# Kernel optimization log

Measured on AMD Instinct MI355X. Metric: run time of the kernel, lower is better.

## Reference

```python
import jax, jax.numpy as jnp
import numpy as np

BN_EPS = 1e-5

def conv1x1(t, w, b):
    # t: [B,Cin,H,W], w: [Cout,Cin], b: [Cout]
    return jnp.einsum('bchw,oc->bohw', t, w) + b[None, :, None, None]

def setup_inputs() -> dict:
    key = jax.random.key(0)
    ks = jax.random.split(key, 11)
    B, Cx, Hx, Wx = 8, 64, 128, 64
    Cy, Hy, Wy = 256, 64, 32
    d = Cy // 8  # num_heads=8
    return {
        'x': jax.random.normal(ks[0], (B, Cx, Hx, Wx), jnp.float32),
        'y': jax.random.normal(ks[1], (B, Cy, Hy, Wy), jnp.float32),
        'wq': jax.random.normal(ks[2], (d, Cy), jnp.float32) * 0.05,
        'bq': jax.random.normal(ks[3], (d,), jnp.float32) * 0.05,
        'wk': jax.random.normal(ks[4], (d, Cy), jnp.float32) * 0.05,
        'bk': jax.random.normal(ks[5], (d,), jnp.float32) * 0.05,
        'wv': jax.random.normal(ks[6], (Cx, Cx), jnp.float32) * 0.05,
        'bv': jax.random.normal(ks[7], (Cx,), jnp.float32) * 0.05,
        'gamma': jax.random.normal(ks[8], (1,), jnp.float32),
        'bn_w': jax.random.normal(ks[9], (Cx,), jnp.float32),
        'bn_b': jax.random.normal(ks[10], (Cx,), jnp.float32),
    }

def reference(x, y, wq, bq, wk, bk, wv, bv, gamma, bn_w, bn_b):
    B, Cx, Hx, Wx = x.shape
    _, Cy, Hy, Wy = y.shape
    size_x = Hx * Wx
    size_y = Hy * Wy
    r = size_x // size_y  # nearest-upsample replication factor (integer here)

    q = conv1x1(y, wq, bq).reshape(B, -1, size_y)  # [B,d,Sy]
    k = conv1x1(y, wk, bk).reshape(B, -1, size_y)  # [B,d,Sy]
    energy = jnp.einsum('bds,bdt->bst', q, k)      # [B,Sy,Sy]
    A = jax.nn.softmax(energy, axis=-1)            # [B,Sy,Sy]

    v = conv1x1(x, wv, bv).reshape(B, Cx, size_x)  # [B,Cx,Sx]
    # Nearest upsample of A to [Sx,Sx] with A_up[i,j]=A[i//r, j//r], then
    # out[c,i] = sum_j v[c,j]*A_up[i,j]  ==  repeat( v_pooled @ A^T , r )
    v_pool = v.reshape(B, Cx, size_y, r).sum(-1)   # block-sum over j within each low-res bin
    O = jnp.einsum('bcj,bij->bci', v_pool, A)      # [B,Cx,Sy]
    out = jnp.repeat(O, r, axis=-1)                # replicate along i: index i -> i//r
    out = out.reshape(B, Cx, Hx, Wx)

    out = gamma[0] * out
    # BatchNorm2d (training-mode batch statistics, biased variance)
    mean = out.mean(axis=(0, 2, 3), keepdims=True)
    var = out.var(axis=(0, 2, 3), keepdims=True)
    out = (out - mean) * jax.lax.rsqrt(var + BN_EPS)
    out = out * bn_w[None, :, None, None] + bn_b[None, :, None, None]
    return x + out
```

## Files before the change

kernel.cpp:

```cpp
#include <hip/hip_runtime.h>
#include <hip/hip_bf16.h>

typedef __attribute__((ext_vector_type(8))) short short8;
typedef __attribute__((ext_vector_type(4))) float f32x4;
typedef unsigned short ushort_t;
typedef unsigned int uint_t;

static constexpr int B  = 8;
static constexpr int CX = 64;
static constexpr int SX = 8192;
static constexpr int CY = 256;
static constexpr int SY = 2048;
static constexpr int D  = 32;

static constexpr size_t OFF_Q  = 0;
static constexpr size_t OFF_K  = OFF_Q + (size_t)B*SY*D*2;
static constexpr size_t OFF_V  = OFF_K + (size_t)B*SY*D*2;
static constexpr size_t OFF_O  = OFF_V + (size_t)B*CX*SY*2;
static constexpr size_t OFF_P1 = OFF_O + (size_t)B*CX*SY*4;
static constexpr size_t OFF_P2 = OFF_P1 + 512*64*4;
static constexpr size_t OFF_SC = OFF_P2 + 512*64*4;
static constexpr size_t OFF_SH = OFF_SC + 64*4;

__device__ inline ushort_t f2bf(float f) {
    uint_t u = __builtin_bit_cast(uint_t, f);
    u += 0x7fffu + ((u >> 16) & 1u);
    return (ushort_t)(u >> 16);
}
__device__ inline uint_t pack_bf16(float a, float b) {
    uint_t ua = __builtin_bit_cast(uint_t, a);
    uint_t ub = __builtin_bit_cast(uint_t, b);
    ua += 0x7fffu + ((ua >> 16) & 1u);
    ub += 0x7fffu + ((ub >> 16) & 1u);
    return (ua >> 16) | (ub & 0xffff0000u);
}

__global__ __launch_bounds__(1024) void k_qk(
    const float* __restrict__ y, const float* __restrict__ wq,
    const float* __restrict__ bq, const float* __restrict__ wk,
    const float* __restrict__ bk, ushort_t* __restrict__ qT, ushort_t* __restrict__ kT)
{
    __shared__ __align__(16) unsigned char Wl[32768];
    __shared__ __align__(16) unsigned char Yl[32768];
    const int t  = threadIdx.x;
    const int b  = blockIdx.x >> 5;
    const int s0 = (blockIdx.x & 31) << 6;

#pragma unroll
    for (int p = 0; p < 8; ++p) {
        const int idx = p * 1024 + t;
        const int o   = idx >> 7;
        const int c2  = idx & 127;
        const float f0 = (o < 32) ? wq[o * CY + 2 * c2]     : wk[(o - 32) * CY + 2 * c2];
        const float f1 = (o < 32) ? wq[o * CY + 2 * c2 + 1] : wk[(o - 32) * CY + 2 * c2 + 1];
        *reinterpret_cast<uint_t*>(Wl + ((o * 512 + c2 * 4) ^ ((o & 7) << 4))) = pack_bf16(f0, f1);
    }
    {
        const int l = t & 63, cg = t >> 6;
        const float* ysrc = y + (size_t)(b * CY + cg * 16) * SY + s0 + l;
#pragma unroll
        for (int k = 0; k < 8; ++k) {
            const float f0 = ysrc[(2 * k)     * SY];
            const float f1 = ysrc[(2 * k + 1) * SY];
            const int c = cg * 16 + 2 * k;
            *reinterpret_cast<uint_t*>(Yl + ((l * 512 + c * 2) ^ ((l & 7) << 4))) = pack_bf16(f0, f1);
        }
    }
    __syncthreads();

    const int w  = t >> 6, l = t & 63;
    const int li = l & 15, g = l >> 4;
    const int ot = w & 3,  st = w >> 2;
    const int oo = ot * 16 + li;
    const int ss = st * 16 + li;

    f32x4 acc = (f32x4){0.f, 0.f, 0.f, 0.f};
#pragma unroll
    for (int ch = 0; ch < 8; ++ch) {
        const short8 wf = *reinterpret_cast<const short8*>(
            Wl + ((oo * 512 + ch * 64 + g * 16) ^ ((oo & 7) << 4)));
        const short8 yf = *reinterpret_cast<const short8*>(
            Yl + ((ss * 512 + ch * 64 + g * 16) ^ ((ss & 7) << 4)));
        acc = __builtin_amdgcn_mfma_f32_16x16x32_bf16(wf, yf, acc, 0, 0, 0);
    }
    const float* bias = (ot < 2) ? bq : bk;
    const int ob = (ot & 1) * 16 + g * 4;
    const float v0 = acc[0] + bias[ob + 0];
    const float v1 = acc[1] + bias[ob + 1];
    const float v2 = acc[2] + bias[ob + 2];
    const float v3 = acc[3] + bias[ob + 3];
    uint2 pw; pw.x = pack_bf16(v0, v1); pw.y = pack_bf16(v2, v3);
    ushort_t* dst = (ot < 2) ? qT : kT;
    *reinterpret_cast<uint2*>(dst + (size_t)(b * SY + s0 + ss) * D + ob) = pw;
}

__global__ __launch_bounds__(1024) void k_v(
    const float* __restrict__ x, const float* __restrict__ wv,
    const float* __restrict__ bv, ushort_t* __restrict__ vB)
{
    __shared__ __align__(16) float xp[64][68];
    __shared__ __align__(16) float wt[64][68];
    const int t   = threadIdx.x;
    const int b   = blockIdx.x >> 5;
    const int jj0 = (blockIdx.x & 31) << 6;

#pragma unroll
    for (int p = 0; p < 4; ++p) {
        const int f = p * 1024 + t;
        const int co = f >> 6, ci = f & 63;
        wt[ci][co] = wv[co * 64 + ci];
    }
    {
        const float4* x4 = reinterpret_cast<const float4*>(x);
#pragma unroll
        for (int p = 0; p < 4; ++p) {
            const int f = p * 1024 + t;
            const int ci = f >> 6, j = f & 63;
            const float4 v = x4[(size_t)(b * CX + ci) * (SX / 4) + jj0 + j];
            xp[ci][j] = (v.x + v.y) + (v.z + v.w);
        }
    }
    __syncthreads();

    const int w = t >> 6, j = t & 63;
    float a0 = 0.f, a1 = 0.f, a2 = 0.f, a3 = 0.f;
#pragma unroll 4
    for (int ci = 0; ci < 64; ++ci) {
        const float xv = xp[ci][j];
        const float4 w4 = *reinterpret_cast<const float4*>(&wt[ci][w * 4]);
        a0 += w4.x * xv; a1 += w4.y * xv; a2 += w4.z * xv; a3 += w4.w * xv;
    }
    const int c0 = w * 4;
    const size_t base = (size_t)(b * CX) * SY + jj0 + j;
    vB[base + (size_t)(c0 + 0) * SY] = f2bf(a0 + 4.f * bv[c0 + 0]);
    vB[base + (size_t)(c0 + 1) * SY] = f2bf(a1 + 4.f * bv[c0 + 1]);
    vB[base + (size_t)(c0 + 2) * SY] = f2bf(a2 + 4.f * bv[c0 + 2]);
    vB[base + (size_t)(c0 + 3) * SY] = f2bf(a3 + 4.f * bv[c0 + 3]);
}

__global__ __launch_bounds__(1024) void k_attn(
    const ushort_t* __restrict__ qT, const ushort_t* __restrict__ kT,
    const ushort_t* __restrict__ vB, float* __restrict__ O,
    float* __restrict__ part1, float* __restrict__ part2)
{
    __shared__ __align__(16) unsigned char smem[65536];
    unsigned char* Kb0 = smem;
    unsigned char* Kb1 = smem + 8192;
    unsigned char* Vb0 = smem + 16384;
    unsigned char* Vb1 = smem + 32768;
    unsigned char* Pl  = smem + 49152;
    float* Otile = reinterpret_cast<float*>(smem);
    float* Lpart = reinterpret_cast<float*>(smem + 17408);
    float* invL  = reinterpret_cast<float*>(smem + 19456);

    const int t  = threadIdx.x;
    const int w  = t >> 6, l = t & 63;
    const int g  = l >> 4, li = l & 15;
    const int b  = blockIdx.x >> 5;
    const int i0 = (blockIdx.x & 31) << 6;

    const int jtt = w >> 1, h = w & 1;
    const int n   = w & 3,  ks = w >> 2;
    const int m0  = 2 * h, m1 = 2 * h + 1;

    const ushort_t* kb = kT + (size_t)b * SY * D;
    const ushort_t* vb = vB + (size_t)b * CX * SY;

    const short8 qf0 = *reinterpret_cast<const short8*>(
        qT + ((size_t)(b * SY + i0 + m0 * 16 + li)) * D + g * 8);
    const short8 qf1 = *reinterpret_cast<const short8*>(
        qT + ((size_t)(b * SY + i0 + m1 * 16 + li)) * D + g * 8);

    const int koff = w * 1024 + l * 16;
    const int vc = w * 4 + g;
    const int vldso = vc * 256 + li * 16;
    const unsigned char* kgb = reinterpret_cast<const unsigned char*>(kb);
    const unsigned char* vgb = reinterpret_cast<const unsigned char*>(vb)
                             + (size_t)vc * (SY * 2) + ((li ^ (vc & 7)) * 16);

    f32x4 acc[4];
#pragma unroll
    for (int m = 0; m < 4; ++m) acc[m] = (f32x4){0.f, 0.f, 0.f, 0.f};
    float lsum0 = 0.f, lsum1 = 0.f;

    const int swzP = (li & 7) << 4;

    {
        short8 kr, vr;
        if (w < 8) kr = *reinterpret_cast<const short8*>(kgb + koff);
        vr = *reinterpret_cast<const short8*>(vgb);
        if (w < 8) *reinterpret_cast<short8*>(Kb0 + koff) = kr;
        *reinterpret_cast<short8*>(Vb0 + vldso) = vr;
    }
    __syncthreads();

    for (int ch = 0; ch < 16; ++ch) {
        unsigned char* Kc = (ch & 1) ? Kb1 : Kb0;
        unsigned char* Vc = (ch & 1) ? Vb1 : Vb0;
        unsigned char* Kn = (ch & 1) ? Kb0 : Kb1;
        unsigned char* Vn = (ch & 1) ? Vb0 : Vb1;

        short8 kr, vr;
        if (ch < 15) {
            if (w < 8) kr = *reinterpret_cast<const short8*>(kgb + (size_t)(ch + 1) * 8192 + koff);
            vr = *reinterpret_cast<const short8*>(vgb + (size_t)(ch + 1) * 256);
        }

        const short8 kf = *reinterpret_cast<const short8*>(Kc + (jtt * 16 + li) * 64 + g * 16);
        const f32x4 d0 = __builtin_amdgcn_mfma_f32_16x16x32_bf16(kf, qf0, (f32x4){0.f,0.f,0.f,0.f}, 0, 0, 0);
        const f32x4 d1 = __builtin_amdgcn_mfma_f32_16x16x32_bf16(kf, qf1, (f32x4){0.f,0.f,0.f,0.f}, 0, 0, 0);

        {
            const float e0 = __expf(d0[0]), e1 = __expf(d0[1]);
            const float e2 = __expf(d0[2]), e3 = __expf(d0[3]);
            lsum0 += (e0 + e1) + (e2 + e3);
            uint2 pw; pw.x = pack_bf16(e0, e1); pw.y = pack_bf16(e2, e3);
            *reinterpret_cast<uint2*>(Pl + (m0 * 16 + li) * 256 + ((jtt * 32 + g * 8) ^ swzP)) = pw;
        }
        {
            const float e0 = __expf(d1[0]), e1 = __expf(d1[1]);
            const float e2 = __expf(d1[2]), e3 = __expf(d1[3]);
            lsum1 += (e0 + e1) + (e2 + e3);
            uint2 pw; pw.x = pack_bf16(e0, e1); pw.y = pack_bf16(e2, e3);
            *reinterpret_cast<uint2*>(Pl + (m1 * 16 + li) * 256 + ((jtt * 32 + g * 8) ^ swzP)) = pw;
        }
        __syncthreads();

        const short8 vf = *reinterpret_cast<const short8*>(
            Vc + (n * 16 + li) * 256 + ((ks * 64 + g * 16) ^ swzP));
#pragma unroll
        for (int m = 0; m < 4; ++m) {
            const short8 pf = *reinterpret_cast<const short8*>(
                Pl + (m * 16 + li) * 256 + ((ks * 64 + g * 16) ^ swzP));
            acc[m] = __builtin_amdgcn_mfma_f32_16x16x32_bf16(pf, vf, acc[m], 0, 0, 0);
        }

        if (ch < 15) {
            if (w < 8) *reinterpret_cast<short8*>(Kn + koff) = kr;
            *reinterpret_cast<short8*>(Vn + vldso) = vr;
        }
        __syncthreads();
    }

    lsum0 += __shfl_xor(lsum0, 16, 64);
    lsum0 += __shfl_xor(lsum0, 32, 64);
    lsum1 += __shfl_xor(lsum1, 16, 64);
    lsum1 += __shfl_xor(lsum1, 32, 64);
    if (l < 16) {
        Lpart[jtt * 64 + m0 * 16 + l] = lsum0;
        Lpart[jtt * 64 + m1 * 16 + l] = lsum1;
    }
    if (ks == 0) {
#pragma unroll
        for (int m = 0; m < 4; ++m) {
            float4 v = make_float4(acc[m][0], acc[m][1], acc[m][2], acc[m][3]);
            *reinterpret_cast<float4*>(&Otile[(n * 16 + li) * 68 + m * 16 + g * 4]) = v;
        }
    }
    __syncthreads();
    if (t < 64) {
        float L = 0.f;
#pragma unroll
        for (int jj = 0; jj < 8; ++jj) L += Lpart[jj * 64 + t];
        invL[t] = 1.f / L;
    }
    if (ks == 1) {
#pragma unroll
        for (int m = 0; m < 4; ++m) {
            float4* p = reinterpret_cast<float4*>(&Otile[(n * 16 + li) * 68 + m * 16 + g * 4]);
            float4 v = *p;
            v.x += acc[m][0]; v.y += acc[m][1]; v.z += acc[m][2]; v.w += acc[m][3];
            *p = v;
        }
    }
    __syncthreads();
    if (ks == 2) {
#pragma unroll
        for (int m = 0; m < 4; ++m) {
            float4* p = reinterpret_cast<float4*>(&Otile[(n * 16 + li) * 68 + m * 16 + g * 4]);
            float4 v = *p;
            v.x += acc[m][0]; v.y += acc[m][1]; v.z += acc[m][2]; v.w += acc[m][3];
            *p = v;
        }
    }
    __syncthreads();
    if (ks == 3) {
#pragma unroll
        for (int m = 0; m < 4; ++m) {
            float4* p = reinterpret_cast<float4*>(&Otile[(n * 16 + li) * 68 + m * 16 + g * 4]);
            float4 v = *p;
            v.x += acc[m][0]; v.y += acc[m][1]; v.z += acc[m][2]; v.w += acc[m][3];
            *p = v;
        }
    }
    __syncthreads();

    if (t < 64) {
        float sa = 0.f, sq = 0.f;
        for (int i = 0; i < 64; ++i) {
            const float v = Otile[t * 68 + i] * invL[i];
            sa += v; sq += v * v;
        }
        part1[blockIdx.x * 64 + t] = sa;
        part2[blockIdx.x * 64 + t] = sq;
    }

    {
        const int c = t >> 4, i4 = t & 15;
        float4 o;
        o.x = Otile[c * 68 + i4 * 4 + 0] * invL[i4 * 4 + 0];
        o.y = Otile[c * 68 + i4 * 4 + 1] * invL[i4 * 4 + 1];
        o.z = Otile[c * 68 + i4 * 4 + 2] * invL[i4 * 4 + 2];
        o.w = Otile[c * 68 + i4 * 4 + 3] * invL[i4 * 4 + 3];
        reinterpret_cast<float4*>(O)[(size_t)(b * CX + c) * (SY / 4) + (i0 >> 2) + i4] = o;
    }
}

__global__ __launch_bounds__(1024) void k_bn(
    const float* __restrict__ part1, const float* __restrict__ part2,
    const float* __restrict__ gamma, const float* __restrict__ bn_w,
    const float* __restrict__ bn_b, float* __restrict__ sc,
    float* __restrict__ sh)
{
    __shared__ float r1[16][64], r2[16][64];
    const int t = threadIdx.x;
    const int c = t & 63, q = t >> 6;
    float s1 = 0.f, s2 = 0.f;
#pragma unroll
    for (int n = 0; n < 16; ++n) {
        const int row = n * 16 + q;
        s1 += part1[row * 64 + c];
        s2 += part2[row * 64 + c];
    }
    r1[q][c] = s1; r2[q][c] = s2;
    __syncthreads();
    if (t < 64) {
        float S1 = 0.f, S2 = 0.f;
#pragma unroll
        for (int k = 0; k < 16; ++k) { S1 += r1[k][t]; S2 += r2[k][t]; }
        const float g = gamma[0];
        const float invN = 1.f / 16384.f;
        const float mean = S1 * invN;
        const float var  = S2 * invN - mean * mean;
        const float inv  = rsqrtf(g * g * var + 1e-5f);
        const float scale = g * inv * bn_w[t];
        sc[t] = scale;
        sh[t] = bn_b[t] - mean * scale;
    }
}

__global__ __launch_bounds__(256) void k_out(
    const float* __restrict__ x, const float* __restrict__ Obuf,
    const float* __restrict__ sc, const float* __restrict__ sh,
    float* __restrict__ out)
{
    const int gid = blockIdx.x * 256 + threadIdx.x;
    const int c = (gid >> 11) & 63;
    const float o  = Obuf[gid];
    const float4 xv = reinterpret_cast<const float4*>(x)[gid];
    const float val = o * sc[c] + sh[c];
    float4 r;
    r.x = xv.x + val; r.y = xv.y + val; r.z = xv.z + val; r.w = xv.w + val;
    reinterpret_cast<float4*>(out)[gid] = r;
}

extern "C" void kernel_launch(void* const* d_in, const int* in_sizes, int n_in,
                              void* d_out, int out_size, void* d_ws, size_t ws_size,
                              hipStream_t stream)
{
    (void)in_sizes; (void)n_in; (void)out_size; (void)ws_size;
    const float* x  = (const float*)d_in[0];
    const float* y  = (const float*)d_in[1];
    const float* wq = (const float*)d_in[2];
    const float* bq = (const float*)d_in[3];
    const float* wk = (const float*)d_in[4];
    const float* bk = (const float*)d_in[5];
    const float* wv = (const float*)d_in[6];
    const float* bv = (const float*)d_in[7];
    const float* gm = (const float*)d_in[8];
    const float* bw = (const float*)d_in[9];
    const float* bb = (const float*)d_in[10];

    char* ws = (char*)d_ws;
    ushort_t* qT  = (ushort_t*)(ws + OFF_Q);
    ushort_t* kT  = (ushort_t*)(ws + OFF_K);
    ushort_t* vBp = (ushort_t*)(ws + OFF_V);
    float*    Ob  = (float*)(ws + OFF_O);
    float*    p1  = (float*)(ws + OFF_P1);
    float*    p2  = (float*)(ws + OFF_P2);
    float*    scp = (float*)(ws + OFF_SC);
    float*    shp = (float*)(ws + OFF_SH);

    k_qk  <<<256, 1024, 0, stream>>>(y, wq, bq, wk, bk, qT, kT);
    k_v   <<<256, 1024, 0, stream>>>(x, wv, bv, vBp);
    k_attn<<<256, 1024, 0, stream>>>(qT, kT, vBp, Ob, p1, p2);
    k_bn  <<<1,   1024, 0, stream>>>(p1, p2, gm, bw, bb, scp, shp);
    k_out <<<4096, 256, 0, stream>>>(x, Ob, scp, shp, (float*)d_out);
}
```

Baseline: 133.2 us.

## Give each wave a private P tile to remove mid-chunk block barrier

```diff
diff --git a/kernel.cpp b/kernel.cpp
--- a/kernel.cpp
+++ b/kernel.cpp
@@ -143,15 +143,15 @@
     const ushort_t* __restrict__ vB, float* __restrict__ O,
     float* __restrict__ part1, float* __restrict__ part2)
 {
-    __shared__ __align__(16) unsigned char smem[65536];
+    __shared__ __align__(16) unsigned char smem[69632];
     unsigned char* Kb0 = smem;
     unsigned char* Kb1 = smem + 8192;
     unsigned char* Vb0 = smem + 16384;
     unsigned char* Vb1 = smem + 32768;
-    unsigned char* Pl  = smem + 49152;
+    unsigned char* Pw  = smem + 49152;
     float* Otile = reinterpret_cast<float*>(smem);
     float* Lpart = reinterpret_cast<float*>(smem + 17408);
-    float* invL  = reinterpret_cast<float*>(smem + 19456);
+    float* invL  = reinterpret_cast<float*>(smem + 18432);
 
     const int t  = threadIdx.x;
     const int w  = t >> 6, l = t & 63;
@@ -159,17 +159,14 @@
     const int b  = blockIdx.x >> 5;
     const int i0 = (blockIdx.x & 31) << 6;
 
-    const int jtt = w >> 1, h = w & 1;
-    const int n   = w & 3,  ks = w >> 2;
-    const int m0  = 2 * h, m1 = 2 * h + 1;
+    const int m  = w & 3;
+    const int jq = w >> 2;
 
     const ushort_t* kb = kT + (size_t)b * SY * D;
     const ushort_t* vb = vB + (size_t)b * CX * SY;
 
-    const short8 qf0 = *reinterpret_cast<const short8*>(
-        qT + ((size_t)(b * SY + i0 + m0 * 16 + li)) * D + g * 8);
-    const short8 qf1 = *reinterpret_cast<const short8*>(
-        qT + ((size_t)(b * SY + i0 + m1 * 16 + li)) * D + g * 8);
+    const short8 qf = *reinterpret_cast<const short8*>(
+        qT + ((size_t)(b * SY + i0 + m * 16 + li)) * D + g * 8);
 
     const int koff = w * 1024 + l * 16;
     const int vc = w * 4 + g;
@@ -178,12 +175,13 @@
     const unsigned char* vgb = reinterpret_cast<const unsigned char*>(vb)
                              + (size_t)vc * (SY * 2) + ((li ^ (vc & 7)) * 16);
 
+    unsigned char* Pme = Pw + w * 1280;
+    const int swzV = (li & 7) << 4;
+
     f32x4 acc[4];
 #pragma unroll
-    for (int m = 0; m < 4; ++m) acc[m] = (f32x4){0.f, 0.f, 0.f, 0.f};
-    float lsum0 = 0.f, lsum1 = 0.f;
-
-    const int swzP = (li & 7) << 4;
+    for (int n = 0; n < 4; ++n) acc[n] = (f32x4){0.f, 0.f, 0.f, 0.f};
+    float lsum = 0.f;
 
     {
         short8 kr, vr;
@@ -206,33 +204,29 @@
             vr = *reinterpret_cast<const short8*>(vgb + (size_t)(ch + 1) * 256);
         }
 
-        const short8 kf = *reinterpret_cast<const short8*>(Kc + (jtt * 16 + li) * 64 + g * 16);
-        const f32x4 d0 = __builtin_amdgcn_mfma_f32_16x16x32_bf16(kf, qf0, (f32x4){0.f,0.f,0.f,0.f}, 0, 0, 0);
-        const f32x4 d1 = __builtin_amdgcn_mfma_f32_16x16x32_bf16(kf, qf1, (f32x4){0.f,0.f,0.f,0.f}, 0, 0, 0);
+        const short8 kf0 = *reinterpret_cast<const short8*>(Kc + (jq * 32 + li) * 64 + g * 16);
+        const short8 kf1 = *reinterpret_cast<const short8*>(Kc + (jq * 32 + 16 + li) * 64 + g * 16);
+        const f32x4 d0 = __builtin_amdgcn_mfma_f32_16x16x32_bf16(kf0, qf, (f32x4){0.f,0.f,0.f,0.f}, 0, 0, 0);
+        const f32x4 d1 = __builtin_amdgcn_mfma_f32_16x16x32_bf16(kf1, qf, (f32x4){0.f,0.f,0.f,0.f}, 0, 0, 0);
 
         {
             const float e0 = __expf(d0[0]), e1 = __expf(d0[1]);
             const float e2 = __expf(d0[2]), e3 = __expf(d0[3]);
-            lsum0 += (e0 + e1) + (e2 + e3);
-            uint2 pw; pw.x = pack_bf16(e0, e1); pw.y = pack_bf16(e2, e3);
-            *reinterpret_cast<uint2*>(Pl + (m0 * 16 + li) * 256 + ((jtt * 32 + g * 8) ^ swzP)) = pw;
-        }
-        {
-            const float e0 = __expf(d1[0]), e1 = __expf(d1[1]);
-            const float e2 = __expf(d1[2]), e3 = __expf(d1[3]);
-            lsum1 += (e0 + e1) + (e2 + e3);
-            uint2 pw; pw.x = pack_bf16(e0, e1); pw.y = pack_bf16(e2, e3);
-            *reinterpret_cast<uint2*>(Pl + (m1 * 16 + li) * 256 + ((jtt * 32 + g * 8) ^ swzP)) = pw;
-        }
-        __syncthreads();
-
-        const short8 vf = *reinterpret_cast<const short8*>(
-            Vc + (n * 16 + li) * 256 + ((ks * 64 + g * 16) ^ swzP));
-#pragma unroll
-        for (int m = 0; m < 4; ++m) {
-            const short8 pf = *reinterpret_cast<const short8*>(
-                Pl + (m * 16 + li) * 256 + ((ks * 64 + g * 16) ^ swzP));
-            acc[m] = __builtin_amdgcn_mfma_f32_16x16x32_bf16(pf, vf, acc[m], 0, 0, 0);
+            const float h0 = __expf(d1[0]), h1 = __expf(d1[1]);
+            const float h2 = __expf(d1[2]), h3 = __expf(d1[3]);
+            lsum += ((e0 + e1) + (e2 + e3)) + ((h0 + h1) + (h2 + h3));
+            uint2 p0; p0.x = pack_bf16(e0, e1); p0.y = pack_bf16(e2, e3);
+            *reinterpret_cast<uint2*>(Pme + li * 80 + 8 * g) = p0;
+            uint2 p1; p1.x = pack_bf16(h0, h1); p1.y = pack_bf16(h2, h3);
+            *reinterpret_cast<uint2*>(Pme + li * 80 + 32 + 8 * g) = p1;
+        }
+
+        const short8 pf = *reinterpret_cast<const short8*>(Pme + li * 80 + 16 * g);
+#pragma unroll
+        for (int n = 0; n < 4; ++n) {
+            const short8 vf = *reinterpret_cast<const short8*>(
+                Vc + (n * 16 + li) * 256 + ((jq * 64 + g * 16) ^ swzV));
+            acc[n] = __builtin_amdgcn_mfma_f32_16x16x32_bf16(pf, vf, acc[n], 0, 0, 0);
         }
 
         if (ch < 15) {
@@ -242,54 +236,50 @@
         __syncthreads();
     }
 
-    lsum0 += __shfl_xor(lsum0, 16, 64);
-    lsum0 += __shfl_xor(lsum0, 32, 64);
-    lsum1 += __shfl_xor(lsum1, 16, 64);
-    lsum1 += __shfl_xor(lsum1, 32, 64);
-    if (l < 16) {
-        Lpart[jtt * 64 + m0 * 16 + l] = lsum0;
-        Lpart[jtt * 64 + m1 * 16 + l] = lsum1;
-    }
-    if (ks == 0) {
-#pragma unroll
-        for (int m = 0; m < 4; ++m) {
-            float4 v = make_float4(acc[m][0], acc[m][1], acc[m][2], acc[m][3]);
-            *reinterpret_cast<float4*>(&Otile[(n * 16 + li) * 68 + m * 16 + g * 4]) = v;
+    lsum += __shfl_xor(lsum, 16, 64);
+    lsum += __shfl_xor(lsum, 32, 64);
+    if (l < 16) Lpart[jq * 64 + m * 16 + l] = lsum;
+
+    if (jq == 0) {
+#pragma unroll
+        for (int n = 0; n < 4; ++n) {
+            *reinterpret_cast<float4*>(&Otile[(n * 16 + li) * 68 + m * 16 + g * 4]) =
+                make_float4(acc[n][0], acc[n][1], acc[n][2], acc[n][3]);
         }
     }
     __syncthreads();
     if (t < 64) {
         float L = 0.f;
 #pragma unroll
-        for (int jj = 0; jj < 8; ++jj) L += Lpart[jj * 64 + t];
+        for (int jj = 0; jj < 4; ++jj) L += Lpart[jj * 64 + t];
         invL[t] = 1.f / L;
     }
-    if (ks == 1) {
-#pragma unroll
-        for (int m = 0; m < 4; ++m) {
+    if (jq == 1) {
+#pragma unroll
+        for (int n = 0; n < 4; ++n) {
             float4* p = reinterpret_cast<float4*>(&Otile[(n * 16 + li) * 68 + m * 16 + g * 4]);
             float4 v = *p;
-            v.x += acc[m][0]; v.y += acc[m][1]; v.z += acc[m][2]; v.w += acc[m][3];
+            v.x += acc[n][0]; v.y += acc[n][1]; v.z += acc[n][2]; v.w += acc[n][3];
             *p = v;
         }
     }
     __syncthreads();
-    if (ks == 2) {
-#pragma unroll
-        for (int m = 0; m < 4; ++m) {
+    if (jq == 2) {
+#pragma unroll
+        for (int n = 0; n < 4; ++n) {
             float4* p = reinterpret_cast<float4*>(&Otile[(n * 16 + li) * 68 + m * 16 + g * 4]);
             float4 v = *p;
-            v.x += acc[m][0]; v.y += acc[m][1]; v.z += acc[m][2]; v.w += acc[m][3];
+            v.x += acc[n][0]; v.y += acc[n][1]; v.z += acc[n][2]; v.w += acc[n][3];
             *p = v;
         }
     }
     __syncthreads();
-    if (ks == 3) {
-#pragma unroll
-        for (int m = 0; m < 4; ++m) {
+    if (jq == 3) {
+#pragma unroll
+        for (int n = 0; n < 4; ++n) {
             float4* p = reinterpret_cast<float4*>(&Otile[(n * 16 + li) * 68 + m * 16 + g * 4]);
             float4 v = *p;
-            v.x += acc[m][0]; v.y += acc[m][1]; v.z += acc[m][2]; v.w += acc[m][3];
+            v.x += acc[n][0]; v.y += acc[n][1]; v.z += acc[n][2]; v.w += acc[n][3];
             *p = v;
         }
     }
```

Result: no change. 131.0 us (-1.6%).
